# Optimization experiments

Measured on AMD Instinct MI355X. Metric: run time of the kernel, lower is better.

The kernel has to match this reference:

```python
import jax, jax.numpy as jnp
import numpy as np

VOCAB, SEQ, HID, HEADS, LAYERS = 30522, 512, 768, 12, 12
DH = HID // HEADS
BATCH = 32
LN_EPS = 1e-12


def setup_inputs() -> dict:
    key = jax.random.key(0)
    ks = jax.random.split(key, 12)
    x = jax.random.randint(ks[0], (BATCH, SEQ), 0, VOCAB)
    word_emb = jax.random.normal(ks[1], (VOCAB, HID), jnp.float32) * 0.02
    pos_emb = jax.random.normal(ks[2], (SEQ, HID), jnp.float32) * 0.02
    type_emb = jax.random.normal(ks[3], (HID,), jnp.float32) * 0.02
    ln_g = jnp.ones((HID,), jnp.float32)
    ln_b = jnp.zeros((HID,), jnp.float32)
    # per-layer mats (original uses torch.ones placeholders; random here for a
    # meaningful correctness baseline, same math)
    W = jax.random.normal(ks[4], (LAYERS, HID, HID), jnp.float32) * 0.02
    b = jax.random.normal(ks[5], (LAYERS, HID), jnp.float32) * 0.02
    M = jax.random.normal(ks[6], (LAYERS, HEADS, SEQ, SEQ), jnp.float32) * (1.0 / np.sqrt(SEQ))
    last_w = jax.random.normal(ks[7], (HID, HID), jnp.float32) * 0.02
    last_b = jax.random.normal(ks[8], (HID,), jnp.float32) * 0.02
    return {"x": x, "word_emb": word_emb, "pos_emb": pos_emb, "type_emb": type_emb,
            "ln_g": ln_g, "ln_b": ln_b, "W": W, "b": b, "M": M,
            "last_w": last_w, "last_b": last_b}


def _layernorm(h, g, beta):
    mu = jnp.mean(h, axis=-1, keepdims=True)
    var = jnp.mean(jnp.square(h - mu), axis=-1, keepdims=True)
    return (h - mu) * jax.lax.rsqrt(var + LN_EPS) * g + beta


def _multihead_mut(h, Mi):
    # original: per (batch, head) loop of (dh, msl) @ (msl, msl).
    # out[b,t,h,d] = sum_s h[b,s,h,d] * M[h,s,t]
    b, s, _ = h.shape
    hx = h.reshape(b, s, HEADS, DH)
    out = jnp.einsum('bshd,hst->bthd', hx, Mi)
    return out.reshape(b, s, HID)


def reference(x, word_emb, pos_emb, type_emb, ln_g, ln_b, W, b, M, last_w, last_b):
    # BertEmbeddings: word + position + token_type(all zeros -> single row) + LayerNorm
    h = word_emb[x] + pos_emb[None, :, :] + type_emb
    h = _layernorm(h, ln_g, ln_b)
    for i in range(LAYERS):
        h = h @ W[i].T                 # [B,S,D]
        h = _multihead_mut(h, M[i])    # per-head seq mixing
        h = jax.nn.relu(h + b[i])
    return h @ last_w.T + last_b
```

## Files before the change

kernel.cpp:

```cpp
#include <hip/hip_runtime.h>
#include <hip/hip_bf16.h>

#define SEQ 512
#define HID 768
#define HEADS 12
#define DH 64
#define LAYERS 12
#define BATCH 32
#define TOK (BATCH*SEQ)
#define NPH (BATCH*DH)

typedef __attribute__((ext_vector_type(8))) __bf16 bf16x8;
typedef __attribute__((ext_vector_type(4))) __bf16 bf16x4;
typedef __attribute__((ext_vector_type(4))) float f32x4;

typedef __attribute__((address_space(1))) const void gvoid;
typedef __attribute__((address_space(3))) void svoid;
__device__ __forceinline__ void async_cp16(const void* g, void* l) {
  __builtin_amdgcn_global_load_lds((gvoid*)g, (svoid*)l, 16, 0, 0);
}

__global__ __launch_bounds__(256) void convert_k(
    const float* __restrict__ src, __bf16* __restrict__ dst) {
  int i = (blockIdx.x * 256 + threadIdx.x) * 4;
  f32x4 v = *(const f32x4*)&src[i];
  bf16x4 b;
#pragma unroll
  for (int j = 0; j < 4; j++) b[j] = (__bf16)v[j];
  *(bf16x4*)&dst[i] = b;
}

__global__ __launch_bounds__(256) void embed_ln_k(
    const int* __restrict__ x, const float* __restrict__ we,
    const float* __restrict__ pe, const float* __restrict__ te,
    const float* __restrict__ g, const float* __restrict__ be,
    __bf16* __restrict__ h) {
  const int tok = blockIdx.x;
  const int s = tok & (SEQ - 1);
  const int wid = x[tok];
  const int tid = threadIdx.x;
  float v[3];
  float sum = 0.f, sq = 0.f;
#pragma unroll
  for (int j = 0; j < 3; j++) {
    int c = tid + j * 256;
    float val = we[(size_t)wid * HID + c] + pe[(size_t)s * HID + c] + te[c];
    v[j] = val; sum += val; sq += val * val;
  }
#pragma unroll
  for (int off = 32; off > 0; off >>= 1) {
    sum += __shfl_down(sum, off);
    sq  += __shfl_down(sq, off);
  }
  __shared__ float rs_[4], rq_[4];
  const int wv = tid >> 6;
  if ((tid & 63) == 0) { rs_[wv] = sum; rq_[wv] = sq; }
  __syncthreads();
  sum = rs_[0] + rs_[1] + rs_[2] + rs_[3];
  sq  = rq_[0] + rq_[1] + rq_[2] + rq_[3];
  const float mu  = sum * (1.f / HID);
  const float var = sq * (1.f / HID) - mu * mu;
  const float inv = rsqrtf(var + 1e-12f);
#pragma unroll
  for (int j = 0; j < 3; j++) {
    int c = tid + j * 256;
    float o = (v[j] - mu) * inv * g[c] + be[c];
    h[(size_t)tok * HID + c] = (__bf16)o;
  }
}

__global__ __launch_bounds__(256) void transpose_all_m_k(
    const float* __restrict__ M, __bf16* __restrict__ Mt) {
  __shared__ float tile[64][68];
  const int lh = blockIdx.z;
  const int t0 = blockIdx.x * 64, s0 = blockIdx.y * 64;
  const float* src = M + (size_t)lh * SEQ * SEQ;
  __bf16* dst = Mt + (size_t)lh * SEQ * SEQ;
  const int tid = threadIdx.x;
#pragma unroll
  for (int it = 0; it < 4; it++) {
    int e = (it * 256 + tid) * 4;
    int r = e >> 6, c = e & 63;
    *(f32x4*)&tile[r][c] = *(const f32x4*)&src[(size_t)(s0 + r) * SEQ + t0 + c];
  }
  __syncthreads();
#pragma unroll
  for (int it = 0; it < 2; it++) {
    int e = (it * 256 + tid) * 8;
    int r = e >> 6, c = e & 63;
    bf16x8 vv;
#pragma unroll
    for (int j = 0; j < 8; j++) vv[j] = (__bf16)tile[c + j][r];
    *(bf16x8*)&dst[(size_t)(t0 + r) * SEQ + s0 + c] = vv;
  }
}

__global__ __launch_bounds__(256) void dense_t_k(
    const __bf16* __restrict__ Wb, const __bf16* __restrict__ hin,
    __bf16* __restrict__ X) {
  __shared__ __bf16 Al[128 * 32];
  __shared__ __bf16 Bl[128 * 32];
  const int n0 = blockIdx.x * 128;
  const int m0 = blockIdx.y * 128;
  const int tid = threadIdx.x;
  const int wave = tid >> 6, lane = tid & 63;
  const int wm = (wave >> 1) << 6, wn = (wave & 1) << 6;
  const int lm = lane & 15, q = lane >> 4;
  const int lrow = lane >> 2, lcol = (lane & 3) * 8;
  f32x4 acc[4][4];
#pragma unroll
  for (int i = 0; i < 4; i++)
#pragma unroll
    for (int j = 0; j < 4; j++) acc[i][j] = {0.f, 0.f, 0.f, 0.f};

  for (int k0 = 0; k0 < HID; k0 += 32) {
#pragma unroll
    for (int it = 0; it < 2; it++) {
      int c = wave * 2 + it;
      int row = c * 16 + lrow;
      async_cp16(&Wb[(size_t)(m0 + row) * HID + k0 + lcol], &Al[c * 512 + lane * 8]);
      async_cp16(&hin[(size_t)(n0 + row) * HID + k0 + lcol], &Bl[c * 512 + lane * 8]);
    }
    __syncthreads();
    bf16x8 af[4], bfr[4];
#pragma unroll
    for (int i = 0; i < 4; i++) {
      af[i]  = *(const bf16x8*)&Al[(wm + i * 16 + lm) * 32 + q * 8];
      bfr[i] = *(const bf16x8*)&Bl[(wn + i * 16 + lm) * 32 + q * 8];
    }
#pragma unroll
    for (int mi = 0; mi < 4; mi++)
#pragma unroll
      for (int ni = 0; ni < 4; ni++)
        acc[mi][ni] = __builtin_amdgcn_mfma_f32_16x16x32_bf16(af[mi], bfr[ni], acc[mi][ni], 0, 0, 0);
    __syncthreads();
  }
#pragma unroll
  for (int mi = 0; mi < 4; mi++)
#pragma unroll
    for (int ni = 0; ni < 4; ni++)
#pragma unroll
      for (int r = 0; r < 4; r++) {
        int dout = m0 + wm + mi * 16 + q * 4 + r;
        int tok  = n0 + wn + ni * 16 + lm;
        int hh = dout >> 6, dd = dout & 63;
        int bb = tok >> 9, ss = tok & (SEQ - 1);
        X[(size_t)hh * (NPH * SEQ) + (size_t)bb * (DH * SEQ) + (size_t)dd * SEQ + ss] =
            (__bf16)acc[mi][ni][r];
      }
}

__global__ __launch_bounds__(256) void mix_relu_k(
    const __bf16* __restrict__ Mtl, const __bf16* __restrict__ X,
    const float* __restrict__ bias_l, __bf16* __restrict__ hout) {
  __shared__ __bf16 Al[128 * 32];
  __shared__ __bf16 Bl[128 * 32];
  const int t0 = blockIdx.x * 128;
  const int n0 = blockIdx.y * 128;
  const int head = blockIdx.z;
  const __bf16* A = Mtl + (size_t)head * SEQ * SEQ;
  const __bf16* B = X + (size_t)head * (NPH * SEQ);
  const int tid = threadIdx.x;
  const int wave = tid >> 6, lane = tid & 63;
  const int wm = (wave >> 1) << 6, wn = (wave & 1) << 6;
  const int lm = lane & 15, q = lane >> 4;
  const int lrow = lane >> 2, lcol = (lane & 3) * 8;
  f32x4 acc[4][4];
#pragma unroll
  for (int i = 0; i < 4; i++)
#pragma unroll
    for (int j = 0; j < 4; j++) acc[i][j] = {0.f, 0.f, 0.f, 0.f};

  for (int k0 = 0; k0 < SEQ; k0 += 32) {
#pragma unroll
    for (int it = 0; it < 2; it++) {
      int c = wave * 2 + it;
      int row = c * 16 + lrow;
      async_cp16(&A[(size_t)(t0 + row) * SEQ + k0 + lcol], &Al[c * 512 + lane * 8]);
      async_cp16(&B[(size_t)(n0 + row) * SEQ + k0 + lcol], &Bl[c * 512 + lane * 8]);
    }
    __syncthreads();
    bf16x8 af[4], bfr[4];
#pragma unroll
    for (int i = 0; i < 4; i++) {
      af[i]  = *(const bf16x8*)&Al[(wm + i * 16 + lm) * 32 + q * 8];
      bfr[i] = *(const bf16x8*)&Bl[(wn + i * 16 + lm) * 32 + q * 8];
    }
#pragma unroll
    for (int mi = 0; mi < 4; mi++)
#pragma unroll
      for (int ni = 0; ni < 4; ni++)
        acc[mi][ni] = __builtin_amdgcn_mfma_f32_16x16x32_bf16(af[mi], bfr[ni], acc[mi][ni], 0, 0, 0);
    __syncthreads();
  }
  const int bb = (n0 + wn) >> 6;
  float bias[4];
#pragma unroll
  for (int ni = 0; ni < 4; ni++) bias[ni] = bias_l[head * DH + ni * 16 + lm];
#pragma unroll
  for (int mi = 0; mi < 4; mi++)
#pragma unroll
    for (int ni = 0; ni < 4; ni++)
#pragma unroll
      for (int r = 0; r < 4; r++) {
        int t = t0 + wm + mi * 16 + q * 4 + r;
        int d = ni * 16 + lm;
        float vv = fmaxf(acc[mi][ni][r] + bias[ni], 0.f);
        hout[((size_t)bb * SEQ + t) * HID + head * DH + d] = (__bf16)vv;
      }
}

__global__ __launch_bounds__(256) void dense_nat_k(
    const __bf16* __restrict__ hin, const __bf16* __restrict__ lwb,
    const float* __restrict__ lb, float* __restrict__ out) {
  __shared__ __bf16 Al[128 * 32];
  __shared__ __bf16 Bl[128 * 32];
  const int m0 = blockIdx.x * 128;
  const int n0 = blockIdx.y * 128;
  const int tid = threadIdx.x;
  const int wave = tid >> 6, lane = tid & 63;
  const int wm = (wave >> 1) << 6, wn = (wave & 1) << 6;
  const int lm = lane & 15, q = lane >> 4;
  const int lrow = lane >> 2, lcol = (lane & 3) * 8;
  f32x4 acc[4][4];
#pragma unroll
  for (int i = 0; i < 4; i++)
#pragma unroll
    for (int j = 0; j < 4; j++) acc[i][j] = {0.f, 0.f, 0.f, 0.f};

  for (int k0 = 0; k0 < HID; k0 += 32) {
#pragma unroll
    for (int it = 0; it < 2; it++) {
      int c = wave * 2 + it;
      int row = c * 16 + lrow;
      async_cp16(&hin[(size_t)(m0 + row) * HID + k0 + lcol], &Al[c * 512 + lane * 8]);
      async_cp16(&lwb[(size_t)(n0 + row) * HID + k0 + lcol], &Bl[c * 512 + lane * 8]);
    }
    __syncthreads();
    bf16x8 af[4], bfr[4];
#pragma unroll
    for (int i = 0; i < 4; i++) {
      af[i]  = *(const bf16x8*)&Al[(wm + i * 16 + lm) * 32 + q * 8];
      bfr[i] = *(const bf16x8*)&Bl[(wn + i * 16 + lm) * 32 + q * 8];
    }
#pragma unroll
    for (int mi = 0; mi < 4; mi++)
#pragma unroll
      for (int ni = 0; ni < 4; ni++)
        acc[mi][ni] = __builtin_amdgcn_mfma_f32_16x16x32_bf16(af[mi], bfr[ni], acc[mi][ni], 0, 0, 0);
    __syncthreads();
  }
#pragma unroll
  for (int mi = 0; mi < 4; mi++)
#pragma unroll
    for (int ni = 0; ni < 4; ni++) {
      float bias = lb[n0 + wn + ni * 16 + lm];
#pragma unroll
      for (int r = 0; r < 4; r++) {
        int tok = m0 + wm + mi * 16 + q * 4 + r;
        int n = n0 + wn + ni * 16 + lm;
        out[(size_t)tok * HID + n] = acc[mi][ni][r] + bias;
      }
    }
}

extern "C" void kernel_launch(void* const* d_in, const int* in_sizes, int n_in,
                              void* d_out, int out_size, void* d_ws, size_t ws_size,
                              hipStream_t stream) {
  const int*   x   = (const int*)d_in[0];
  const float* we  = (const float*)d_in[1];
  const float* pe  = (const float*)d_in[2];
  const float* te  = (const float*)d_in[3];
  const float* lng = (const float*)d_in[4];
  const float* lnb = (const float*)d_in[5];
  const float* W   = (const float*)d_in[6];
  const float* bb  = (const float*)d_in[7];
  const float* M   = (const float*)d_in[8];
  const float* lw  = (const float*)d_in[9];
  const float* lb  = (const float*)d_in[10];

  __bf16* Mt  = (__bf16*)d_ws;
  __bf16* Wb  = Mt + (size_t)LAYERS * HEADS * SEQ * SEQ;
  __bf16* lwb = Wb + (size_t)LAYERS * HID * HID;
  __bf16* hA  = lwb + (size_t)HID * HID;
  __bf16* X   = hA + (size_t)TOK * HID;
  float* out = (float*)d_out;

  convert_k<<<LAYERS * HID * HID / 1024, 256, 0, stream>>>(W, Wb);
  convert_k<<<HID * HID / 1024, 256, 0, stream>>>(lw, lwb);
  transpose_all_m_k<<<dim3(8, 8, LAYERS * HEADS), 256, 0, stream>>>(M, Mt);
  embed_ln_k<<<TOK, 256, 0, stream>>>(x, we, pe, te, lng, lnb, hA);
  for (int l = 0; l < LAYERS; l++) {
    dense_t_k<<<dim3(TOK / 128, HID / 128), 256, 0, stream>>>(Wb + (size_t)l * HID * HID, hA, X);
    mix_relu_k<<<dim3(SEQ / 128, NPH / 128, HEADS), 256, 0, stream>>>(
        Mt + (size_t)l * HEADS * SEQ * SEQ, X, bb + (size_t)l * HID, hA);
  }
  dense_nat_k<<<dim3(TOK / 128, HID / 128), 256, 0, stream>>>(hA, lwb, lb, out);
}
```

Measured before the change: 1.027 ms.

## Replace three GEMM kernels with unified 256x256 double-buffered pipelined MFMA kernel

Result: slower. 1.405 ms (+36.8%).

```diff
diff --git a/kernel.cpp b/kernel.cpp
--- a/kernel.cpp
+++ b/kernel.cpp
@@ -19,6 +19,11 @@
 __device__ __forceinline__ void async_cp16(const void* g, void* l) {
   __builtin_amdgcn_global_load_lds((gvoid*)g, (svoid*)l, 16, 0, 0);
 }
+
+#define SB   __builtin_amdgcn_s_barrier()
+#define FENCE asm volatile("" ::: "memory")
+#define LGKM0 do { asm volatile("s_waitcnt lgkmcnt(0)" ::: "memory"); \
+                   __builtin_amdgcn_sched_barrier(0); } while (0)
 
 __global__ __launch_bounds__(256) void convert_k(
     const float* __restrict__ src, __bf16* __restrict__ dst) {
@@ -95,173 +100,150 @@
   }
 }
 
-__global__ __launch_bounds__(256) void dense_t_k(
-    const __bf16* __restrict__ Wb, const __bf16* __restrict__ hin,
-    __bf16* __restrict__ X) {
-  __shared__ __bf16 Al[128 * 32];
-  __shared__ __bf16 Bl[128 * 32];
-  const int n0 = blockIdx.x * 128;
-  const int m0 = blockIdx.y * 128;
+template <int MODE>
+__global__ __launch_bounds__(512, 2) void gemm256_k(
+    const __bf16* __restrict__ Abase, const __bf16* __restrict__ Bbase,
+    const float* __restrict__ bias, void* __restrict__ Cout, int K) {
+  __shared__ __bf16 LA[2][2][128 * 64];
+  __shared__ __bf16 LB[2][2][128 * 64];
   const int tid = threadIdx.x;
-  const int wave = tid >> 6, lane = tid & 63;
-  const int wm = (wave >> 1) << 6, wn = (wave & 1) << 6;
+  const int w = tid >> 6, lane = tid & 63;
   const int lm = lane & 15, q = lane >> 4;
-  const int lrow = lane >> 2, lcol = (lane & 3) * 8;
-  f32x4 acc[4][4];
-#pragma unroll
-  for (int i = 0; i < 4; i++)
+  const int srow = lane >> 3;
+  const int scol = ((lane & 7) * 8) ^ ((lane & 32) ? 16 : 0);
+  const int axor = (lm & 4) ? 16 : 0;
+  const int haA = w >> 2;
+  const int hbB = (w & 3) >> 1;
+  const int rB0 = (w & 1) * 64;
+  const int m0 = blockIdx.x * 256, n0 = blockIdx.y * 256;
+  const __bf16* A = Abase;
+  const __bf16* B = Bbase;
+  int head = 0;
+  if constexpr (MODE == 1) {
+    head = blockIdx.z;
+    A += (size_t)head * SEQ * SEQ;
+    B += (size_t)head * (NPH * SEQ);
+  }
+
+  auto STAGE = [&](int jt, int h, int isB) {
+    const __bf16* src = isB ? B : A;
+    const int r0 = (isB ? n0 : m0) + h * 128 + w * 16 + srow;
+    const int kc = jt * 64 + scol;
+    __bf16* lds = (isB ? &LB[jt & 1][h][0] : &LA[jt & 1][h][0]) + w * 1024 + lane * 8;
+    async_cp16(&src[(size_t)r0 * K + kc], lds);
+    async_cp16(&src[(size_t)(r0 + 8) * K + kc], lds + 512);
+  };
+
+  f32x4 acc[8][4];
+#pragma unroll
+  for (int i = 0; i < 8; i++)
 #pragma unroll
     for (int j = 0; j < 4; j++) acc[i][j] = {0.f, 0.f, 0.f, 0.f};
 
-  for (int k0 = 0; k0 < HID; k0 += 32) {
-#pragma unroll
-    for (int it = 0; it < 2; it++) {
-      int c = wave * 2 + it;
-      int row = c * 16 + lrow;
-      async_cp16(&Wb[(size_t)(m0 + row) * HID + k0 + lcol], &Al[c * 512 + lane * 8]);
-      async_cp16(&hin[(size_t)(n0 + row) * HID + k0 + lcol], &Bl[c * 512 + lane * 8]);
-    }
-    __syncthreads();
-    bf16x8 af[4], bfr[4];
-#pragma unroll
-    for (int i = 0; i < 4; i++) {
-      af[i]  = *(const bf16x8*)&Al[(wm + i * 16 + lm) * 32 + q * 8];
-      bfr[i] = *(const bf16x8*)&Bl[(wn + i * 16 + lm) * 32 + q * 8];
-    }
-#pragma unroll
-    for (int mi = 0; mi < 4; mi++)
-#pragma unroll
-      for (int ni = 0; ni < 4; ni++)
-        acc[mi][ni] = __builtin_amdgcn_mfma_f32_16x16x32_bf16(af[mi], bfr[ni], acc[mi][ni], 0, 0, 0);
-    __syncthreads();
-  }
-#pragma unroll
-  for (int mi = 0; mi < 4; mi++)
+  const int NT = K >> 6;
+  STAGE(0, 0, 0); STAGE(0, 1, 0);
+  STAGE(0, 0, 1); STAGE(0, 1, 1);
+  STAGE(1, 0, 0); STAGE(1, 1, 0);
+  asm volatile("s_waitcnt vmcnt(4)" ::: "memory");
+  SB; FENCE;
+
+  for (int j = 0; j < NT; ++j) {
+    const __bf16* lA = &LA[j & 1][haA][0];
+    const __bf16* lB = &LB[j & 1][hbB][0];
+    bf16x8 aA[4][2], aB[4][2], b0[2][2], b1[2][2];
+#pragma unroll
+    for (int mi = 0; mi < 4; mi++)
+#pragma unroll
+      for (int ks = 0; ks < 2; ks++)
+        aA[mi][ks] = *(const bf16x8*)&lA[((mi * 16 + lm) * 64 + ks * 32 + q * 8) ^ axor];
+#pragma unroll
+    for (int nn = 0; nn < 2; nn++)
+#pragma unroll
+      for (int ks = 0; ks < 2; ks++)
+        b0[nn][ks] = *(const bf16x8*)&lB[((rB0 + nn * 16 + lm) * 64 + ks * 32 + q * 8) ^ axor];
+    if (j + 1 < NT) STAGE(j + 1, 0, 1);
+    SB; LGKM0;
+    __builtin_amdgcn_s_setprio(1);
+#pragma unroll
+    for (int mi = 0; mi < 4; mi++)
+#pragma unroll
+      for (int nn = 0; nn < 2; nn++)
+#pragma unroll
+        for (int ks = 0; ks < 2; ks++)
+          acc[mi][nn] = __builtin_amdgcn_mfma_f32_16x16x32_bf16(aA[mi][ks], b0[nn][ks], acc[mi][nn], 0, 0, 0);
+    __builtin_amdgcn_s_setprio(0);
+    SB; FENCE;
+#pragma unroll
+    for (int mi = 0; mi < 4; mi++)
+#pragma unroll
+      for (int ks = 0; ks < 2; ks++)
+        aB[mi][ks] = *(const bf16x8*)&lA[(((mi + 4) * 16 + lm) * 64 + ks * 32 + q * 8) ^ axor];
+    if (j + 1 < NT) STAGE(j + 1, 1, 1);
+    SB; LGKM0;
+    __builtin_amdgcn_s_setprio(1);
+#pragma unroll
+    for (int mi = 0; mi < 4; mi++)
+#pragma unroll
+      for (int nn = 0; nn < 2; nn++)
+#pragma unroll
+        for (int ks = 0; ks < 2; ks++)
+          acc[mi + 4][nn] = __builtin_amdgcn_mfma_f32_16x16x32_bf16(aB[mi][ks], b0[nn][ks], acc[mi + 4][nn], 0, 0, 0);
+    __builtin_amdgcn_s_setprio(0);
+    SB; FENCE;
+#pragma unroll
+    for (int nn = 0; nn < 2; nn++)
+#pragma unroll
+      for (int ks = 0; ks < 2; ks++)
+        b1[nn][ks] = *(const bf16x8*)&lB[((rB0 + (nn + 2) * 16 + lm) * 64 + ks * 32 + q * 8) ^ axor];
+    if (j + 2 < NT) STAGE(j + 2, 0, 0);
+    SB; LGKM0;
+    __builtin_amdgcn_s_setprio(1);
+#pragma unroll
+    for (int mi = 0; mi < 4; mi++)
+#pragma unroll
+      for (int nn = 0; nn < 2; nn++)
+#pragma unroll
+        for (int ks = 0; ks < 2; ks++)
+          acc[mi][nn + 2] = __builtin_amdgcn_mfma_f32_16x16x32_bf16(aA[mi][ks], b1[nn][ks], acc[mi][nn + 2], 0, 0, 0);
+    __builtin_amdgcn_s_setprio(0);
+    SB; FENCE;
+    if (j + 2 < NT) STAGE(j + 2, 1, 0);
+    __builtin_amdgcn_s_setprio(1);
+#pragma unroll
+    for (int mi = 0; mi < 4; mi++)
+#pragma unroll
+      for (int nn = 0; nn < 2; nn++)
+#pragma unroll
+        for (int ks = 0; ks < 2; ks++)
+          acc[mi + 4][nn + 2] = __builtin_amdgcn_mfma_f32_16x16x32_bf16(aB[mi][ks], b1[nn][ks], acc[mi + 4][nn + 2], 0, 0, 0);
+    __builtin_amdgcn_s_setprio(0);
+    if (j + 2 < NT) { asm volatile("s_waitcnt vmcnt(4)" ::: "memory"); }
+    else            { asm volatile("s_waitcnt vmcnt(0)" ::: "memory"); }
+    SB; FENCE;
+  }
+
+#pragma unroll
+  for (int mi = 0; mi < 8; mi++)
 #pragma unroll
     for (int ni = 0; ni < 4; ni++)
 #pragma unroll
       for (int r = 0; r < 4; r++) {
-        int dout = m0 + wm + mi * 16 + q * 4 + r;
-        int tok  = n0 + wn + ni * 16 + lm;
-        int hh = dout >> 6, dd = dout & 63;
-        int bb = tok >> 9, ss = tok & (SEQ - 1);
-        X[(size_t)hh * (NPH * SEQ) + (size_t)bb * (DH * SEQ) + (size_t)dd * SEQ + ss] =
-            (__bf16)acc[mi][ni][r];
+        const int row = m0 + (w >> 2) * 128 + mi * 16 + q * 4 + r;
+        const int col = n0 + (w & 3) * 64 + ni * 16 + lm;
+        const float v = acc[mi][ni][r];
+        if constexpr (MODE == 0) {
+          const int hh = row >> 6, dd = row & 63;
+          const int bb2 = col >> 9, ss = col & (SEQ - 1);
+          ((__bf16*)Cout)[(size_t)hh * (NPH * SEQ) + (size_t)bb2 * (DH * SEQ) +
+                          (size_t)dd * SEQ + ss] = (__bf16)v;
+        } else if constexpr (MODE == 1) {
+          const int bb2 = col >> 6, dd = col & 63;
+          const float vv = fmaxf(v + bias[head * DH + dd], 0.f);
+          ((__bf16*)Cout)[((size_t)bb2 * SEQ + row) * HID + head * DH + dd] = (__bf16)vv;
+        } else {
+          ((float*)Cout)[(size_t)row * HID + col] = v + bias[col];
+        }
       }
-}
-
-__global__ __launch_bounds__(256) void mix_relu_k(
-    const __bf16* __restrict__ Mtl, const __bf16* __restrict__ X,
-    const float* __restrict__ bias_l, __bf16* __restrict__ hout) {
-  __shared__ __bf16 Al[128 * 32];
-  __shared__ __bf16 Bl[128 * 32];
-  const int t0 = blockIdx.x * 128;
-  const int n0 = blockIdx.y * 128;
-  const int head = blockIdx.z;
-  const __bf16* A = Mtl + (size_t)head * SEQ * SEQ;
-  const __bf16* B = X + (size_t)head * (NPH * SEQ);
-  const int tid = threadIdx.x;
-  const int wave = tid >> 6, lane = tid & 63;
-  const int wm = (wave >> 1) << 6, wn = (wave & 1) << 6;
-  const int lm = lane & 15, q = lane >> 4;
-  const int lrow = lane >> 2, lcol = (lane & 3) * 8;
-  f32x4 acc[4][4];
-#pragma unroll
-  for (int i = 0; i < 4; i++)
-#pragma unroll
-    for (int j = 0; j < 4; j++) acc[i][j] = {0.f, 0.f, 0.f, 0.f};
-
-  for (int k0 = 0; k0 < SEQ; k0 += 32) {
-#pragma unroll
-    for (int it = 0; it < 2; it++) {
-      int c = wave * 2 + it;
-      int row = c * 16 + lrow;
-      async_cp16(&A[(size_t)(t0 + row) * SEQ + k0 + lcol], &Al[c * 512 + lane * 8]);
-      async_cp16(&B[(size_t)(n0 + row) * SEQ + k0 + lcol], &Bl[c * 512 + lane * 8]);
-    }
-    __syncthreads();
-    bf16x8 af[4], bfr[4];
-#pragma unroll
-    for (int i = 0; i < 4; i++) {
-      af[i]  = *(const bf16x8*)&Al[(wm + i * 16 + lm) * 32 + q * 8];
-      bfr[i] = *(const bf16x8*)&Bl[(wn + i * 16 + lm) * 32 + q * 8];
-    }
-#pragma unroll
-    for (int mi = 0; mi < 4; mi++)
-#pragma unroll
-      for (int ni = 0; ni < 4; ni++)
-        acc[mi][ni] = __builtin_amdgcn_mfma_f32_16x16x32_bf16(af[mi], bfr[ni], acc[mi][ni], 0, 0, 0);
-    __syncthreads();
-  }
-  const int bb = (n0 + wn) >> 6;
-  float bias[4];
-#pragma unroll
-  for (int ni = 0; ni < 4; ni++) bias[ni] = bias_l[head * DH + ni * 16 + lm];
-#pragma unroll
-  for (int mi = 0; mi < 4; mi++)
-#pragma unroll
-    for (int ni = 0; ni < 4; ni++)
-#pragma unroll
-      for (int r = 0; r < 4; r++) {
-        int t = t0 + wm + mi * 16 + q * 4 + r;
-        int d = ni * 16 + lm;
-        float vv = fmaxf(acc[mi][ni][r] + bias[ni], 0.f);
-        hout[((size_t)bb * SEQ + t) * HID + head * DH + d] = (__bf16)vv;
-      }
-}
-
-__global__ __launch_bounds__(256) void dense_nat_k(
-    const __bf16* __restrict__ hin, const __bf16* __restrict__ lwb,
-    const float* __restrict__ lb, float* __restrict__ out) {
-  __shared__ __bf16 Al[128 * 32];
-  __shared__ __bf16 Bl[128 * 32];
-  const int m0 = blockIdx.x * 128;
-  const int n0 = blockIdx.y * 128;
-  const int tid = threadIdx.x;
-  const int wave = tid >> 6, lane = tid & 63;
-  const int wm = (wave >> 1) << 6, wn = (wave & 1) << 6;
-  const int lm = lane & 15, q = lane >> 4;
-  const int lrow = lane >> 2, lcol = (lane & 3) * 8;
-  f32x4 acc[4][4];
-#pragma unroll
-  for (int i = 0; i < 4; i++)
-#pragma unroll
-    for (int j = 0; j < 4; j++) acc[i][j] = {0.f, 0.f, 0.f, 0.f};
-
-  for (int k0 = 0; k0 < HID; k0 += 32) {
-#pragma unroll
-    for (int it = 0; it < 2; it++) {
-      int c = wave * 2 + it;
-      int row = c * 16 + lrow;
-      async_cp16(&hin[(size_t)(m0 + row) * HID + k0 + lcol], &Al[c * 512 + lane * 8]);
-      async_cp16(&lwb[(size_t)(n0 + row) * HID + k0 + lcol], &Bl[c * 512 + lane * 8]);
-    }
-    __syncthreads();
-    bf16x8 af[4], bfr[4];
-#pragma unroll
-    for (int i = 0; i < 4; i++) {
-      af[i]  = *(const bf16x8*)&Al[(wm + i * 16 + lm) * 32 + q * 8];
-      bfr[i] = *(const bf16x8*)&Bl[(wn + i * 16 + lm) * 32 + q * 8];
-    }
-#pragma unroll
-    for (int mi = 0; mi < 4; mi++)
-#pragma unroll
-      for (int ni = 0; ni < 4; ni++)
-        acc[mi][ni] = __builtin_amdgcn_mfma_f32_16x16x32_bf16(af[mi], bfr[ni], acc[mi][ni], 0, 0, 0);
-    __syncthreads();
-  }
-#pragma unroll
-  for (int mi = 0; mi < 4; mi++)
-#pragma unroll
-    for (int ni = 0; ni < 4; ni++) {
-      float bias = lb[n0 + wn + ni * 16 + lm];
-#pragma unroll
-      for (int r = 0; r < 4; r++) {
-        int tok = m0 + wm + mi * 16 + q * 4 + r;
-        int n = n0 + wn + ni * 16 + lm;
-        out[(size_t)tok * HID + n] = acc[mi][ni][r] + bias;
-      }
-    }
 }
 
 extern "C" void kernel_launch(void* const* d_in, const int* in_sizes, int n_in,
@@ -291,9 +273,10 @@
   transpose_all_m_k<<<dim3(8, 8, LAYERS * HEADS), 256, 0, stream>>>(M, Mt);
   embed_ln_k<<<TOK, 256, 0, stream>>>(x, we, pe, te, lng, lnb, hA);
   for (int l = 0; l < LAYERS; l++) {
-    dense_t_k<<<dim3(TOK / 128, HID / 128), 256, 0, stream>>>(Wb + (size_t)l * HID * HID, hA, X);
-    mix_relu_k<<<dim3(SEQ / 128, NPH / 128, HEADS), 256, 0, stream>>>(
-        Mt + (size_t)l * HEADS * SEQ * SEQ, X, bb + (size_t)l * HID, hA);
-  }
-  dense_nat_k<<<dim3(TOK / 128, HID / 128), 256, 0, stream>>>(hA, lwb, lb, out);
-}
+    gemm256_k<0><<<dim3(3, 64), 512, 0, stream>>>(Wb + (size_t)l * HID * HID, hA,
+                                                  nullptr, X, HID);
+    gemm256_k<1><<<dim3(2, 8, HEADS), 512, 0, stream>>>(Mt + (size_t)l * HEADS * SEQ * SEQ, X,
+                                                        bb + (size_t)l * HID, hA, SEQ);
+  }
+  gemm256_k<2><<<dim3(64, 3), 512, 0, stream>>>(hA, lwb, lb, out, HID);
+}
```
